# Performance work log

Hardware: AMD Instinct MI355X
Metric: run time of the kernel (lower is better)

## Reference

```python
import jax, jax.numpy as jnp
import numpy as np

CHANNELS = 64

def setup_inputs() -> dict:
    key = jax.random.key(0)
    k1, k2, k3, k4, k5, k6, k7 = jax.random.split(key, 7)
    N, E = 100000, 1200000
    x = jax.random.normal(k1, (N, CHANNELS), dtype=jnp.float32)
    sources = jax.random.randint(k2, (E,), 0, N, dtype=jnp.int64)
    targets = jax.random.randint(k3, (E,), 0, N, dtype=jnp.int64)
    norm = jax.random.uniform(k4, (N, 1), dtype=jnp.float32)
    norm_t = jax.random.uniform(k5, (N, 1), dtype=jnp.float32)
    # xavier_normal_ for a [64,64] weight: std = sqrt(2/(64+64))
    std = float(np.sqrt(2.0 / (CHANNELS + CHANNELS)))
    w_out = jax.random.normal(k6, (CHANNELS, CHANNELS), dtype=jnp.float32) * std
    w_back = jax.random.normal(k7, (CHANNELS, CHANNELS), dtype=jnp.float32) * std
    return {"x": x, "sources": sources, "targets": targets,
            "norm": norm, "norm_t": norm_t, "w_out": w_out, "w_back": w_back}

def _conv(x, src, tgt, norm, weight):
    # out-of-place index_add: x + scatter_add(x[src] -> tgt), then norm scale, then matmul
    agg = x.at[tgt].add(x[src])          # [N, C]
    return (norm * agg) @ weight         # [N, C]

def reference(x, sources, targets, norm, norm_t, w_out, w_back):
    out = _conv(x, sources, targets, norm, w_out)
    back = _conv(x, targets, sources, norm_t, w_back)
    return out + back
```

## Files before the change

### kernel.cpp

```cpp
#include <hip/hip_runtime.h>
#include <hip/hip_fp16.h>


constexpr int C = 64;
constexpr int SLOT = 40;
constexpr int STRIDE = 48;

__device__ __forceinline__ float lane_bcast(float v, int k) {
    return __int_as_float(__builtin_amdgcn_readlane(__float_as_int(v), k));
}

__global__ void cvt_kernel(const float2* __restrict__ xf2,
                           __half2* __restrict__ xh2z, int N) {
    int stride = gridDim.x * blockDim.x;
    int total = (N + 1) * 32;
    for (int i = blockIdx.x * blockDim.x + threadIdx.x; i < total; i += stride) {
        int row = i >> 5, j = i & 31;
        if (row == 0) {
            xh2z[i] = __floats2half2_rn(0.f, 0.f);
        } else {
            float2 v = xf2[(size_t)(row - 1) * 32 + j];
            xh2z[i] = __floats2half2_rn(v.x, v.y);
        }
    }
}

__global__ void hist_place_kernel(const int* __restrict__ src,
                                  const int* __restrict__ tgt,
                                  int* __restrict__ cnt,
                                  int* __restrict__ ebufA,
                                  int* __restrict__ ebufB,
                                  int N, int E) {
    int stride = gridDim.x * blockDim.x;
    for (int e = blockIdx.x * blockDim.x + threadIdx.x; e < E; e += stride) {
        int t_ = tgt[e];
        int s_ = src[e];
        int rA = atomicAdd(&cnt[t_], 1);
        if (rA < SLOT) atomicAdd(&ebufA[t_ * STRIDE + rA], s_ + 1);
        int rB = atomicAdd(&cnt[N + s_], 1);
        if (rB < SLOT) atomicAdd(&ebufB[s_ * STRIDE + rB], t_ + 1);
    }
}

__global__ __launch_bounds__(256)
void gather_ell_kernel(const __half2* __restrict__ xh2z,
                       const int* __restrict__ cnt,
                       int* __restrict__ ebufA,
                       int* __restrict__ ebufB,
                       int N) {
    int lane = threadIdx.x & 63;
    int h = lane >> 5;
    int j = lane & 31;
    int wave = blockIdx.x * (blockDim.x >> 6) + (threadIdx.x >> 6);
    int wstride = (blockDim.x >> 6) * gridDim.x;

    for (int n = wave; n < N; n += wstride) {
        int* ra = ebufA + (size_t)n * STRIDE;
        int* rb = ebufB + (size_t)n * STRIDE;
        int dA = min(cnt[n], SLOT);
        int dB = min(cnt[N + n], SLOT);
        int dmax = max(dA, dB);
        float axA = 0.f, ayA = 0.f, axB = 0.f, ayB = 0.f;

        for (int i = 0; i < dmax; i += 8) {
            if (i < dA) {
                int i0 = ra[i + h],     i1 = ra[i + 2 + h];
                int i2 = ra[i + 4 + h], i3 = ra[i + 6 + h];
                float2 v0 = __half22float2(xh2z[(size_t)i0 * 32 + j]);
                float2 v1 = __half22float2(xh2z[(size_t)i1 * 32 + j]);
                float2 v2 = __half22float2(xh2z[(size_t)i2 * 32 + j]);
                float2 v3 = __half22float2(xh2z[(size_t)i3 * 32 + j]);
                axA += (v0.x + v1.x) + (v2.x + v3.x);
                ayA += (v0.y + v1.y) + (v2.y + v3.y);
            }
            if (i < dB) {
                int i0 = rb[i + h],     i1 = rb[i + 2 + h];
                int i2 = rb[i + 4 + h], i3 = rb[i + 6 + h];
                float2 v0 = __half22float2(xh2z[(size_t)i0 * 32 + j]);
                float2 v1 = __half22float2(xh2z[(size_t)i1 * 32 + j]);
                float2 v2 = __half22float2(xh2z[(size_t)i2 * 32 + j]);
                float2 v3 = __half22float2(xh2z[(size_t)i3 * 32 + j]);
                axB += (v0.x + v1.x) + (v2.x + v3.x);
                ayB += (v0.y + v1.y) + (v2.y + v3.y);
            }
        }
        axA += __shfl_xor(axA, 32, 64);
        ayA += __shfl_xor(ayA, 32, 64);
        axB += __shfl_xor(axB, 32, 64);
        ayB += __shfl_xor(ayB, 32, 64);
        if (h == 0) {
            ((__half2*)ra)[j] = __floats2half2_rn(axA, ayA);
            ((__half2*)rb)[j] = __floats2half2_rn(axB, ayB);
        }
    }
}

__global__ __launch_bounds__(256, 2)
void fused_mm_kernel(const float* __restrict__ x,
                     const int* __restrict__ ebufA,
                     const int* __restrict__ ebufB,
                     const float* __restrict__ norm,
                     const float* __restrict__ norm_t,
                     const float* __restrict__ w_out,
                     const float* __restrict__ w_back,
                     float* __restrict__ out,
                     int N) {
    int lane = threadIdx.x & 63;
    int waveInBlock = threadIdx.x >> 6;
    int wavesTotal = (blockDim.x >> 6) * gridDim.x;
    int waveId = blockIdx.x * (blockDim.x >> 6) + waveInBlock;

    float wo[C], wb[C];
#pragma unroll
    for (int k = 0; k < C; ++k) {
        wo[k] = w_out[k * C + lane];
        wb[k] = w_back[k * C + lane];
    }

    for (int r = waveId; r < N; r += wavesTotal) {
        float xv = x[(size_t)r * C + lane];
        const __half* aggA = (const __half*)(ebufA + (size_t)r * STRIDE);
        const __half* aggB = (const __half*)(ebufB + (size_t)r * STRIDE);
        float aA = xv + __half2float(aggA[lane]);
        float aB = xv + __half2float(aggB[lane]);
        float nm = norm[r];
        float nt = norm_t[r];
        float accA = 0.f, accB = 0.f;
#pragma unroll
        for (int k = 0; k < C; ++k) {
            accA = fmaf(lane_bcast(aA, k), wo[k], accA);
            accB = fmaf(lane_bcast(aB, k), wb[k], accB);
        }
        out[(size_t)r * C + lane] = nm * accA + nt * accB;
    }
}

extern "C" void kernel_launch(void* const* d_in, const int* in_sizes, int n_in,
                              void* d_out, int out_size, void* d_ws, size_t ws_size,
                              hipStream_t stream) {
    const float* x      = (const float*)d_in[0];
    const int*   src    = (const int*)d_in[1];
    const int*   tgt    = (const int*)d_in[2];
    const float* norm   = (const float*)d_in[3];
    const float* norm_t = (const float*)d_in[4];
    const float* w_out  = (const float*)d_in[5];
    const float* w_back = (const float*)d_in[6];
    float* out = (float*)d_out;

    int N = in_sizes[0] / C;
    int E = in_sizes[1];

    __half2* xh2z = (__half2*)d_ws;
    int* cnt   = (int*)(xh2z + (size_t)(N + 1) * 32);
    int* ebufA = cnt + 2 * N;
    int* ebufB = ebufA + (size_t)N * STRIDE;

    cvt_kernel<<<2048, 256, 0, stream>>>((const float2*)x, xh2z, N);

    hipMemsetAsync(cnt, 0, (size_t)(2 * N + 2 * (size_t)N * STRIDE) * sizeof(int), stream);

    hist_place_kernel<<<(E + 255) / 256, 256, 0, stream>>>(src, tgt, cnt, ebufA, ebufB, N, E);

    gather_ell_kernel<<<2048, 256, 0, stream>>>(xh2z, cnt, ebufA, ebufB, N);

    fused_mm_kernel<<<1024, 256, 0, stream>>>(x, ebufA, ebufB, norm, norm_t,
                                              w_out, w_back, out, N);
}
```

Baseline: 332.8 us.

## Split edge histogram and placement into two passes with padded counters

The fused histogram-and-place kernel becomes two kernels. The first does the per-node counter atomics, spacing counters 32 bytes apart, and stores each edge's two ranks packed as bytes in a ushort array. The second reads those ranks back and writes the neighbour indices into the ELL buffers. The ELL row stride also drops from 48 to 40 ints, which shrinks the buffers and the memset. The aim is to cut false sharing and contention between the counter atomics and the scattered ELL writes. The cost is an extra pass over the edge arrays, a larger counter region to clear, and ranks that wrap if a node's degree exceeds 255.

```diff
diff --git a/kernel.cpp b/kernel.cpp
--- a/kernel.cpp
+++ b/kernel.cpp
@@ -4,7 +4,8 @@
 
 constexpr int C = 64;
 constexpr int SLOT = 40;
-constexpr int STRIDE = 48;
+constexpr int STRIDE = 40;
+constexpr int PADC = 8;
 
 __device__ __forceinline__ float lane_bcast(float v, int k) {
     return __int_as_float(__builtin_amdgcn_readlane(__float_as_int(v), k));
@@ -25,26 +26,42 @@
     }
 }
 
-__global__ void hist_place_kernel(const int* __restrict__ src,
-                                  const int* __restrict__ tgt,
-                                  int* __restrict__ cnt,
-                                  int* __restrict__ ebufA,
-                                  int* __restrict__ ebufB,
-                                  int N, int E) {
-    int stride = gridDim.x * blockDim.x;
-    for (int e = blockIdx.x * blockDim.x + threadIdx.x; e < E; e += stride) {
+__global__ void hist_rank_kernel(const int* __restrict__ src,
+                                 const int* __restrict__ tgt,
+                                 int* __restrict__ cntp,
+                                 unsigned short* __restrict__ rankp,
+                                 int N, int E) {
+    int e = blockIdx.x * blockDim.x + threadIdx.x;
+    if (e < E) {
         int t_ = tgt[e];
         int s_ = src[e];
-        int rA = atomicAdd(&cnt[t_], 1);
-        if (rA < SLOT) atomicAdd(&ebufA[t_ * STRIDE + rA], s_ + 1);
-        int rB = atomicAdd(&cnt[N + s_], 1);
-        if (rB < SLOT) atomicAdd(&ebufB[s_ * STRIDE + rB], t_ + 1);
+        int rA = atomicAdd(&cntp[(size_t)t_ * PADC], 1);
+        int rB = atomicAdd(&cntp[(size_t)(N + s_) * PADC], 1);
+        rankp[e] = (unsigned short)((rA & 255) | ((rB & 255) << 8));
+    }
+}
+
+__global__ void place_kernel(const int* __restrict__ src,
+                             const int* __restrict__ tgt,
+                             const unsigned short* __restrict__ rankp,
+                             int* __restrict__ ebufA,
+                             int* __restrict__ ebufB,
+                             int N, int E) {
+    int e = blockIdx.x * blockDim.x + threadIdx.x;
+    if (e < E) {
+        int t_ = tgt[e];
+        int s_ = src[e];
+        unsigned r = rankp[e];
+        int rA = r & 255;
+        int rB = r >> 8;
+        if (rA < SLOT) atomicAdd(&ebufA[(size_t)t_ * STRIDE + rA], s_ + 1);
+        if (rB < SLOT) atomicAdd(&ebufB[(size_t)s_ * STRIDE + rB], t_ + 1);
     }
 }
 
 __global__ __launch_bounds__(256)
 void gather_ell_kernel(const __half2* __restrict__ xh2z,
-                       const int* __restrict__ cnt,
+                       const int* __restrict__ cntp,
                        int* __restrict__ ebufA,
                        int* __restrict__ ebufB,
                        int N) {
@@ -57,8 +74,8 @@
     for (int n = wave; n < N; n += wstride) {
         int* ra = ebufA + (size_t)n * STRIDE;
         int* rb = ebufB + (size_t)n * STRIDE;
-        int dA = min(cnt[n], SLOT);
-        int dB = min(cnt[N + n], SLOT);
+        int dA = min(cntp[(size_t)n * PADC], SLOT);
+        int dB = min(cntp[(size_t)(N + n) * PADC], SLOT);
         int dmax = max(dA, dB);
         float axA = 0.f, ayA = 0.f, axB = 0.f, ayB = 0.f;
 
@@ -151,17 +168,22 @@
     int E = in_sizes[1];
 
     __half2* xh2z = (__half2*)d_ws;
-    int* cnt   = (int*)(xh2z + (size_t)(N + 1) * 32);
-    int* ebufA = cnt + 2 * N;
+    int* cntp  = (int*)(xh2z + (size_t)(N + 1) * 32);
+    int* ebufA = cntp + (size_t)2 * N * PADC;
     int* ebufB = ebufA + (size_t)N * STRIDE;
+    unsigned short* rankp = (unsigned short*)(ebufB + (size_t)N * STRIDE);
 
     cvt_kernel<<<2048, 256, 0, stream>>>((const float2*)x, xh2z, N);
 
-    hipMemsetAsync(cnt, 0, (size_t)(2 * N + 2 * (size_t)N * STRIDE) * sizeof(int), stream);
+    hipMemsetAsync(cntp, 0,
+                   ((size_t)2 * N * PADC + (size_t)2 * N * STRIDE) * sizeof(int),
+                   stream);
 
-    hist_place_kernel<<<(E + 255) / 256, 256, 0, stream>>>(src, tgt, cnt, ebufA, ebufB, N, E);
+    hist_rank_kernel<<<(E + 255) / 256, 256, 0, stream>>>(src, tgt, cntp, rankp, N, E);
 
-    gather_ell_kernel<<<2048, 256, 0, stream>>>(xh2z, cnt, ebufA, ebufB, N);
+    place_kernel<<<(E + 255) / 256, 256, 0, stream>>>(src, tgt, rankp, ebufA, ebufB, N, E);
+
+    gather_ell_kernel<<<2048, 256, 0, stream>>>(xh2z, cntp, ebufA, ebufB, N);
 
     fused_mm_kernel<<<1024, 256, 0, stream>>>(x, ebufA, ebufB, norm, norm_t,
                                               w_out, w_back, out, N);
```

New measurement: 304.3 us. 8.6% less time.
